# Optimization experiments

Measured on AMD Instinct MI355X. Metric: run time of the kernel, lower is better.

## Reference

```python
import jax, jax.numpy as jnp
import numpy as np

BS, N, HID, INPUT, PREK, KHOP = 16, 1024, 64, 64, 4, 3
D = 2 * HID            # hidden channel dim (128)
F = 2 * INPUT          # input feature dim (128)
C = F + D              # graphconv input channels (256)
NM = KHOP + 1          # num_metrics = k_hop*n_supports + 1 with n_supports=1
PI = 3.141592653589793
EMB_RANGE = (12.0 + 2.0) / HID   # (gamma + epsilon) / hidden_size


def setup_inputs() -> dict:
    key = jax.random.key(0)
    ks = jax.random.split(key, 12)
    inputs = jax.random.normal(ks[0], (BS, N, F), jnp.float32)
    # per-sample dynamic support; scale by 1/N to keep Chebyshev recursion stable
    supports = jax.random.uniform(ks[1], (BS, N, N), jnp.float32) / N
    hidden_states = jax.random.normal(ks[2], (BS, PREK, N, D), jnp.float32)
    W = jax.random.normal(ks[3], (D, D), jnp.float32) * 0.02
    b = jax.random.normal(ks[4], (N, D), jnp.float32) * 0.02
    R = jax.random.normal(ks[5], (PREK, N, HID), jnp.float32) * 0.02
    gc_w = jax.random.normal(ks[6], (D, C * NM), jnp.float32) * 0.02
    gc_b = jax.random.normal(ks[7], (D,), jnp.float32) * 0.02
    ev_att_w = jax.random.normal(ks[8], (1, N * D), jnp.float32) * 0.001
    ev_att_b = jax.random.normal(ks[9], (1,), jnp.float32) * 0.02
    att_w = jax.random.normal(ks[10], (1, N * D), jnp.float32) * 0.001
    att_b = jax.random.normal(ks[11], (1,), jnp.float32) * 0.02
    return {"inputs": inputs, "supports": supports, "hidden_states": hidden_states,
            "W": W, "b": b, "R": R, "gc_w": gc_w, "gc_b": gc_b,
            "ev_att_w": ev_att_w, "ev_att_b": ev_att_b,
            "att_w": att_w, "att_b": att_b}


def reference(inputs, supports, hidden_states, W, b, R, gc_w, gc_b,
              ev_att_w, ev_att_b, att_w, att_b):
    bs, k, n, d = hidden_states.shape
    # split inputs / last hidden into real/imag halves
    re_in, im_in = jnp.split(inputs, 2, axis=-1)          # [bs,n,INPUT]
    preH = hidden_states[:, -1]                           # [bs,n,d]
    re_p, im_p = jnp.split(preH, 2, axis=-1)              # [bs,n,HID]
    conv_in = jnp.concatenate([re_in, re_p, im_in, im_p], axis=-1)  # [bs,n,C]

    # diffusion graph conv (Chebyshev-style recursion over single batched support)
    x0 = conv_in
    x1 = jnp.matmul(supports, x0)                         # [bs,n,C]
    xs = [x0, x1]
    for _ in range(2, KHOP + 1):
        x2 = 2.0 * jnp.matmul(supports, x1) - x0
        xs.append(x2)
        x0, x1 = x1, x2
    # stack K metrics, permute to [bs,n,C,K], flatten (channel-major, step-minor)
    x = jnp.stack(xs, axis=0).transpose(1, 2, 3, 0).reshape(bs, n, C * NM)
    gco = x @ gc_w.T + gc_b                               # [bs,n,d]

    # EvolutionCell attention over g=1 group (kept for faithfulness)
    xe = gco.reshape(bs, 1, n * d)
    se = xe @ ev_att_w.T + ev_att_b                       # [bs,1,1]
    we = jax.nn.softmax(se, axis=1)
    conv_out = (xe * we).sum(axis=1).reshape(bs, n, d)

    # leaky_relu_ (slope 0.01)
    conv_out = jnp.where(conv_out >= 0, conv_out, 0.01 * conv_out)

    # RotatE-style complex phase rotation of hidden states
    phase = R / (EMB_RANGE / PI)                          # [k,n,HID]
    re_rel, im_rel = jnp.cos(phase), jnp.sin(phase)
    re_h, im_h = jnp.split(hidden_states, 2, axis=-1)     # [bs,k,n,HID]
    re_new = re_rel * re_h - im_rel * im_h
    im_new = im_rel * re_h + re_rel * im_h
    new_states = jnp.concatenate([re_new, im_new], axis=-1)  # [bs,k,n,d]

    # attention over k memory slots
    xa = new_states.reshape(bs, k, n * d)
    sa = xa @ att_w.T + att_b                             # [bs,k,1]
    wa = jax.nn.softmax(sa, axis=1)
    att = (xa * wa).sum(axis=1).reshape(bs, n, d)

    output = conv_out @ W + b[None] + att                 # [bs,n,d]
    new_hidden = jnp.concatenate([hidden_states[:, 1:], output[:, None]], axis=1)
    return output, new_hidden
```

## Files before the change

### kernel.cpp

```cpp
#include <hip/hip_runtime.h>
#include <cstddef>

constexpr float PHASE_SCALE = (float)(3.141592653589793 / ((12.0 + 2.0) / 64.0));

typedef __bf16 bf16;
typedef __bf16 bf16x4 __attribute__((ext_vector_type(4)));
typedef __bf16 bf16x8 __attribute__((ext_vector_type(8)));
typedef float floatx4 __attribute__((ext_vector_type(4)));

#define GLOAD_LDS16(gp, lp) __builtin_amdgcn_global_load_lds( \
    (const __attribute__((address_space(1))) void*)(gp),      \
    (__attribute__((address_space(3))) void*)(lp), 16, 0, 0)

__global__ __launch_bounds__(256) void prep_kernel(
    const float4* __restrict__ S, bf16* __restrict__ Sbf,
    const float* __restrict__ R,
    const float* __restrict__ gcw, const float* __restrict__ W,
    bf16* __restrict__ gtAll, bf16* __restrict__ WT,
    const float* __restrict__ inp, const float* __restrict__ hs,
    bf16* __restrict__ xRow, bf16* __restrict__ xT0,
    const float* __restrict__ attw, float* __restrict__ part)
{
    __shared__ bf16 tile[64][65];
    __shared__ float red[256];
    const int bid = blockIdx.x;
    const int tid = threadIdx.x;

    if (bid < 576) {
        int gi = bid * 256 + tid;
        if (gi < 131072) {
            int m = gi >> 15;
            int rem = gi & 32767;
            int d = rem >> 8;
            int c = rem & 255;
            gtAll[gi] = (bf16)gcw[(size_t)d * 1024 + c * 4 + m];
        } else {
            int r = gi - 131072;
            int n = r >> 7, k = r & 127;
            WT[r] = (bf16)W[(size_t)k * 128 + n];
        }
    } else if (bid < 1088) {
        int bid3 = bid - 576;
        int bk = bid3 & 63;
        int k = bk & 3;
        int chunk = bid3 >> 6;
        const float* hbase = hs + (size_t)bk * 131072;
        float acc = 0.f;
        for (int idx = tid; idx < 2048; idx += 256) {
            int h4 = (idx & 15) * 4;
            int n = chunk * 128 + (idx >> 4);
            float4 rr  = *(const float4*)(R + (size_t)k * 65536 + n * 64 + h4);
            float4 re  = *(const float4*)(hbase + (size_t)n * 128 + h4);
            float4 im  = *(const float4*)(hbase + (size_t)n * 128 + 64 + h4);
            float4 wre = *(const float4*)(attw + (size_t)n * 128 + h4);
            float4 wim = *(const float4*)(attw + (size_t)n * 128 + 64 + h4);
            float sv, cv;
            __sincosf(rr.x * PHASE_SCALE, &sv, &cv);
            acc += (cv * re.x - sv * im.x) * wre.x + (sv * re.x + cv * im.x) * wim.x;
            __sincosf(rr.y * PHASE_SCALE, &sv, &cv);
            acc += (cv * re.y - sv * im.y) * wre.y + (sv * re.y + cv * im.y) * wim.y;
            __sincosf(rr.z * PHASE_SCALE, &sv, &cv);
            acc += (cv * re.z - sv * im.z) * wre.z + (sv * re.z + cv * im.z) * wim.z;
            __sincosf(rr.w * PHASE_SCALE, &sv, &cv);
            acc += (cv * re.w - sv * im.w) * wre.w + (sv * re.w + cv * im.w) * wim.w;
        }
        red[tid] = acc;
        __syncthreads();
        for (int s2 = 128; s2 > 0; s2 >>= 1) {
            if (tid < s2) red[tid] += red[tid + s2];
            __syncthreads();
        }
        if (tid == 0) part[bk * 8 + chunk] = red[0];
    } else if (bid < 2112) {
        int bid2 = bid - 1088;
        int b = bid2 >> 6;
        int by = (bid2 >> 2) & 15;
        int bx = bid2 & 3;
        int n0 = by * 64, c0 = bx * 64;
        #pragma unroll
        for (int it = 0; it < 16; ++it) {
            int idx = it * 256 + tid;
            int cl = idx & 63, nl = idx >> 6;
            int n = n0 + nl, c = c0 + cl;
            const float* irow = inp + ((size_t)b * 1024 + n) * 128;
            const float* prow = hs + (((size_t)b * 4 + 3) * 1024 + n) * 128;
            float v;
            if (c < 64)       v = irow[c];
            else if (c < 128) v = prow[c - 64];
            else if (c < 192) v = irow[c - 64];
            else              v = prow[c - 128];
            bf16 vb = (bf16)v;
            xRow[((size_t)b * 1024 + n) * 256 + c] = vb;
            tile[nl][cl] = vb;
        }
        __syncthreads();
        #pragma unroll
        for (int it = 0; it < 16; ++it) {
            int idx = it * 256 + tid;
            int nl = idx & 63, cl = idx >> 6;
            xT0[((size_t)b * 256 + c0 + cl) * 1024 + n0 + nl] = tile[nl][cl];
        }
    } else {
        int gi = (bid - 2112) * 256 + tid;
        const float4* Sp = S + (size_t)gi * 2;
        float4 v0 = Sp[0];
        float4 v1 = Sp[1];
        bf16x8 o;
        o[0] = (bf16)v0.x; o[1] = (bf16)v0.y; o[2] = (bf16)v0.z; o[3] = (bf16)v0.w;
        o[4] = (bf16)v1.x; o[5] = (bf16)v1.y; o[6] = (bf16)v1.z; o[7] = (bf16)v1.w;
        *(bf16x8*)(Sbf + (size_t)gi * 8) = o;
    }
}

__global__ __launch_bounds__(512) void cheb_mfma_kernel(
    const bf16* __restrict__ S, const bf16* __restrict__ xT,
    const bf16* __restrict__ xTprev, bf16* __restrict__ outT,
    const bf16* __restrict__ xRow0, const bf16* __restrict__ gtA,
    const bf16* __restrict__ gt0, float* __restrict__ gcoF,
    float alpha, int accumulate)
{
    __shared__ char smem[81920];
    const int f = blockIdx.x;
    const int b = (f & 7) + 8 * ((f >> 3) & 1);
    const int n0 = (f >> 4) * 64;
    const int tid = threadIdx.x;
    const int wave = tid >> 6, lane = tid & 63;
    const int wr = (wave & 3) * 16;
    const int wc = (wave >> 2) * 128;
    const int l15 = lane & 15, quad = lane >> 4;
    const int lrow = lane >> 3;
    const int segsw = (lane & 7) ^ lrow;

    const bf16* Sb = S + (size_t)b * 1048576;
    const bf16* xb = xT + (size_t)b * 262144;

    auto stage = [&](int p, int k0) {
        bf16* dA = (bf16*)(smem + p * 40960);
        bf16* dB = dA + 4096;
        {
            const bf16* gp = Sb + (size_t)(n0 + wave * 8 + lrow) * 1024 + k0 + segsw * 8;
            GLOAD_LDS16(gp, dA + wave * 8 * 64);
        }
        #pragma unroll
        for (int v = 0; v < 4; ++v) {
            int cq = wave * 32 + v * 8;
            const bf16* gp = xb + (size_t)(cq + lrow) * 1024 + k0 + segsw * 8;
            GLOAD_LDS16(gp, dB + cq * 64);
        }
    };

    floatx4 acc[8] = {};
    stage(0, 0);
    int p = 0;
    for (int k0 = 0; k0 < 1024; k0 += 64) {
        __syncthreads();
        if (k0 + 64 < 1024) stage(p ^ 1, k0 + 64);
        const bf16* lA = (const bf16*)(smem + p * 40960);
        const bf16* lB = lA + 4096;
        #pragma unroll
        for (int ks = 0; ks < 2; ++ks) {
            int row = wr + l15;
            int aslot = (ks * 4 + quad) ^ (row & 7);
            bf16x8 af = *(const bf16x8*)(lA + row * 64 + aslot * 8);
            #pragma unroll
            for (int j = 0; j < 8; ++j) {
                int col = wc + j * 16 + l15;
                int bslot = (ks * 4 + quad) ^ (col & 7);
                bf16x8 bfr = *(const bf16x8*)(lB + col * 64 + bslot * 8);
                acc[j] = __builtin_amdgcn_mfma_f32_16x16x32_bf16(af, bfr, acc[j], 0, 0, 0);
            }
        }
        p ^= 1;
    }

    const bf16* pT = xTprev ? xTprev + (size_t)b * 262144 : nullptr;
    bf16* oT = outT ? outT + (size_t)b * 262144 : nullptr;
    bf16x4 xo[8];
    #pragma unroll
    for (int j = 0; j < 8; ++j) {
        int col = wc + j * 16 + l15;
        float v[4];
        #pragma unroll
        for (int r = 0; r < 4; ++r) v[r] = alpha * acc[j][r];
        if (pT) {
            bf16x4 pp = *(const bf16x4*)(pT + (size_t)col * 1024 + n0 + wr + quad * 4);
            #pragma unroll
            for (int r = 0; r < 4; ++r) v[r] -= (float)pp[r];
        }
        #pragma unroll
        for (int r = 0; r < 4; ++r) xo[j][r] = (bf16)v[r];
        if (oT) *(bf16x4*)(oT + (size_t)col * 1024 + n0 + wr + quad * 4) = xo[j];
    }

    __syncthreads();
    bf16* ldsX = (bf16*)smem;
    #pragma unroll
    for (int j = 0; j < 8; ++j) {
        int col = wc + j * 16 + l15;
        #pragma unroll
        for (int r = 0; r < 4; ++r)
            ldsX[(wr + quad * 4 + r) * 264 + col] = xo[j][r];
    }
    __syncthreads();

    const int dbase = (wave >> 2) * 64;
    floatx4 a2[4] = {};
    for (int k2 = 0; k2 < 256; k2 += 32) {
        bf16x8 af = *(const bf16x8*)(ldsX + (wr + l15) * 264 + k2 + quad * 8);
        #pragma unroll
        for (int j = 0; j < 4; ++j) {
            int dcol = dbase + j * 16 + l15;
            bf16x8 bfr = *(const bf16x8*)(gtA + (size_t)dcol * 256 + k2 + quad * 8);
            a2[j] = __builtin_amdgcn_mfma_f32_16x16x32_bf16(af, bfr, a2[j], 0, 0, 0);
        }
    }
    if (xRow0) {
        for (int k2 = 0; k2 < 256; k2 += 32) {
            bf16x8 af = *(const bf16x8*)(xRow0 + ((size_t)b * 1024 + n0 + wr + l15) * 256 + k2 + quad * 8);
            #pragma unroll
            for (int j = 0; j < 4; ++j) {
                int dcol = dbase + j * 16 + l15;
                bf16x8 bfr = *(const bf16x8*)(gt0 + (size_t)dcol * 256 + k2 + quad * 8);
                a2[j] = __builtin_amdgcn_mfma_f32_16x16x32_bf16(af, bfr, a2[j], 0, 0, 0);
            }
        }
    }
    #pragma unroll
    for (int j = 0; j < 4; ++j) {
        int dcol = dbase + j * 16 + l15;
        #pragma unroll
        for (int r = 0; r < 4; ++r) {
            size_t idx = ((size_t)b * 1024 + n0 + wr + quad * 4 + r) * 128 + dcol;
            if (accumulate) gcoF[idx] += a2[j][r];
            else            gcoF[idx]  = a2[j][r];
        }
    }
}

__global__ __launch_bounds__(256) void final_kernel(
    const float* __restrict__ gcoF, const float* __restrict__ gcb,
    const bf16* __restrict__ WT, const float* __restrict__ bvec,
    const float* __restrict__ hs, const float* __restrict__ R,
    const float* __restrict__ part, const float* __restrict__ attb,
    float* __restrict__ out, float* __restrict__ newh)
{
    const int m0 = blockIdx.x * 64;
    const int b = m0 >> 10, n0 = m0 & 1023;
    const int tid = threadIdx.x;
    const int wave = tid >> 6, lane = tid & 63;
    const int l15 = lane & 15, quad = lane >> 4;

    const int arow = m0 + wave * 16 + l15;
    floatx4 acc[8] = {};
    #pragma unroll
    for (int k0 = 0; k0 < 128; k0 += 32) {
        int kk = k0 + quad * 8;
        float4 p0 = *(const float4*)(gcoF + (size_t)arow * 128 + kk);
        float4 p1 = *(const float4*)(gcoF + (size_t)arow * 128 + kk + 4);
        float4 g0 = *(const float4*)(gcb + kk);
        float4 g1 = *(const float4*)(gcb + kk + 4);
        float vv[8] = {p0.x + g0.x, p0.y + g0.y, p0.z + g0.z, p0.w + g0.w,
                       p1.x + g1.x, p1.y + g1.y, p1.z + g1.z, p1.w + g1.w};
        bf16x8 af;
        #pragma unroll
        for (int e = 0; e < 8; ++e) {
            float v = vv[e];
            af[e] = (bf16)(v >= 0.f ? v : 0.01f * v);
        }
        #pragma unroll
        for (int j = 0; j < 8; ++j) {
            bf16x8 bfr = *(const bf16x8*)(WT + (size_t)(j * 16 + l15) * 128 + kk);
            acc[j] = __builtin_amdgcn_mfma_f32_16x16x32_bf16(af, bfr, acc[j], 0, 0, 0);
        }
    }

    float sa[4], mx = -1e30f;
    #pragma unroll
    for (int k = 0; k < 4; ++k) {
        float s = attb[0];
        #pragma unroll
        for (int c = 0; c < 8; ++c) s += part[(b * 4 + k) * 8 + c];
        sa[k] = s;
        mx = fmaxf(mx, s);
    }
    float den = 0.f;
    #pragma unroll
    for (int k = 0; k < 4; ++k) { sa[k] = __expf(sa[k] - mx); den += sa[k]; }
    float inv = 1.f / den;
    #pragma unroll
    for (int k = 0; k < 4; ++k) sa[k] *= inv;

    #pragma unroll
    for (int jj = 0; jj < 4; ++jj) {
        int hcol = jj * 16 + l15;
        #pragma unroll
        for (int r = 0; r < 4; ++r) {
            int n = n0 + wave * 16 + quad * 4 + r;
            float attRe = 0.f, attIm = 0.f;
            #pragma unroll
            for (int k = 0; k < 4; ++k) {
                const float* hb = hs + (((size_t)(b * 4 + k) * 1024 + n) * 128);
                float re = hb[hcol], im = hb[64 + hcol];
                float s, c;
                __sincosf(R[(size_t)k * 65536 + n * 64 + hcol] * PHASE_SCALE, &s, &c);
                attRe += sa[k] * (c * re - s * im);
                attIm += sa[k] * (s * re + c * im);
                if (k >= 1) {
                    size_t nb = (size_t)b * 524288 + (size_t)(k - 1) * 131072 + (size_t)n * 128;
                    newh[nb + hcol] = re;
                    newh[nb + 64 + hcol] = im;
                }
            }
            size_t ob = (size_t)(m0 + wave * 16 + quad * 4 + r) * 128;
            float oRe = acc[jj][r]     + bvec[(size_t)n * 128 + hcol]      + attRe;
            float oIm = acc[jj + 4][r] + bvec[(size_t)n * 128 + 64 + hcol] + attIm;
            out[ob + hcol] = oRe;
            out[ob + 64 + hcol] = oIm;
            size_t nb3 = (size_t)b * 524288 + 393216 + (size_t)n * 128;
            newh[nb3 + hcol] = oRe;
            newh[nb3 + 64 + hcol] = oIm;
        }
    }
}

extern "C" void kernel_launch(void* const* d_in, const int* in_sizes, int n_in,
                              void* d_out, int out_size, void* d_ws, size_t ws_size,
                              hipStream_t stream) {
    const float* inp  = (const float*)d_in[0];
    const float* sup  = (const float*)d_in[1];
    const float* hs   = (const float*)d_in[2];
    const float* W    = (const float*)d_in[3];
    const float* bvec = (const float*)d_in[4];
    const float* R    = (const float*)d_in[5];
    const float* gcw  = (const float*)d_in[6];
    const float* gcb  = (const float*)d_in[7];
    const float* attw = (const float*)d_in[10];
    const float* attb = (const float*)d_in[11];

    float* out  = (float*)d_out;
    float* newh = out + 2097152;
    bf16*  Sbf  = (bf16*)newh;

    char* w = (char*)d_ws;
    bf16*  xT0   = (bf16*)(w);
    bf16*  xT1   = (bf16*)(w + 8388608);
    bf16*  xT2   = (bf16*)(w + 16777216);
    bf16*  xRow  = (bf16*)(w + 25165824);
    float* gcoF  = (float*)(w + 33554432);
    bf16*  gtAll = (bf16*)(w + 41943040);
    bf16*  WT    = (bf16*)(w + 42205184);
    float* part  = (float*)(w + 42237952);

    prep_kernel<<<10304, 256, 0, stream>>>((const float4*)sup, Sbf, R, gcw, W,
                                           gtAll, WT, inp, hs, xRow, xT0, attw, part);

    cheb_mfma_kernel<<<256, 512, 0, stream>>>(Sbf, xT0, nullptr, xT1,
                                              xRow, gtAll + 32768, gtAll, gcoF, 1.0f, 0);
    cheb_mfma_kernel<<<256, 512, 0, stream>>>(Sbf, xT1, xT0, xT2,
                                              nullptr, gtAll + 2 * 32768, nullptr, gcoF, 2.0f, 1);
    cheb_mfma_kernel<<<256, 512, 0, stream>>>(Sbf, xT2, xT1, nullptr,
                                              nullptr, gtAll + 3 * 32768, nullptr, gcoF, 2.0f, 1);

    final_kernel<<<256, 256, 0, stream>>>(gcoF, gcb, WT, bvec, hs, R, part, attb, out, newh);
}
```

Measured before the change: 264.9 us.

## Restructure prep kernel: vectorized concat/transpose, fused S conversion into all blocks

Shrinks the prep kernel grid from 10304 to 2048 blocks. Every block now converts four chunks of the support matrix to bf16, and the concat/transpose, attention-score and weight-conversion roles are interleaved across blocks. The input concat is rewritten to load float4 pairs and store bf16x8 rows, with the transposed write emitted as bf16x4, replacing scalar per-element loads and stores. The aim is better memory coalescing and less launch overhead, at the cost of heavier, less uniform per-block work.

```diff
diff --git a/kernel.cpp b/kernel.cpp
--- a/kernel.cpp
+++ b/kernel.cpp
@@ -26,24 +26,42 @@
     const int bid = blockIdx.x;
     const int tid = threadIdx.x;
 
-    if (bid < 576) {
-        int gi = bid * 256 + tid;
-        if (gi < 131072) {
-            int m = gi >> 15;
-            int rem = gi & 32767;
-            int d = rem >> 8;
-            int c = rem & 255;
-            gtAll[gi] = (bf16)gcw[(size_t)d * 1024 + c * 4 + m];
-        } else {
-            int r = gi - 131072;
-            int n = r >> 7, k = r & 127;
-            WT[r] = (bf16)W[(size_t)k * 128 + n];
-        }
-    } else if (bid < 1088) {
-        int bid3 = bid - 576;
-        int bk = bid3 & 63;
+    const int lin = ((bid >> 4) << 3) | (bid & 7);
+
+    if (((bid >> 3) & 1) == 0) {
+        int b = lin >> 6, by = (lin >> 2) & 15, bx = lin & 3;
+        int n0 = by * 64, c0 = bx * 64;
+        const float* base = (bx & 1) ? (hs + (((size_t)b * 4 + 3) * 1024) * 128)
+                                     : (inp + ((size_t)b * 1024) * 128);
+        int soff = (bx >> 1) * 64;
+        #pragma unroll
+        for (int it = 0; it < 2; ++it) {
+            int unit = it * 256 + tid;
+            int nl = unit >> 3, cs = unit & 7;
+            const float* src = base + (size_t)(n0 + nl) * 128 + soff + cs * 8;
+            float4 a0 = *(const float4*)src;
+            float4 a1 = *(const float4*)(src + 4);
+            bf16x8 o;
+            o[0] = (bf16)a0.x; o[1] = (bf16)a0.y; o[2] = (bf16)a0.z; o[3] = (bf16)a0.w;
+            o[4] = (bf16)a1.x; o[5] = (bf16)a1.y; o[6] = (bf16)a1.z; o[7] = (bf16)a1.w;
+            *(bf16x8*)(xRow + ((size_t)b * 1024 + n0 + nl) * 256 + c0 + cs * 8) = o;
+            #pragma unroll
+            for (int e = 0; e < 8; ++e) tile[nl][cs * 8 + e] = o[e];
+        }
+        __syncthreads();
+        #pragma unroll
+        for (int it = 0; it < 4; ++it) {
+            int unit = it * 256 + tid;
+            int ng = unit & 15, cc = unit >> 4;
+            bf16x4 v;
+            #pragma unroll
+            for (int r = 0; r < 4; ++r) v[r] = tile[ng * 4 + r][cc];
+            *(bf16x4*)(xT0 + ((size_t)b * 256 + c0 + cc) * 1024 + n0 + ng * 4) = v;
+        }
+    } else if (lin < 512) {
+        int bk = lin & 63;
         int k = bk & 3;
-        int chunk = bid3 >> 6;
+        int chunk = lin >> 6;
         const float* hbase = hs + (size_t)bk * 131072;
         float acc = 0.f;
         for (int idx = tid; idx < 2048; idx += 256) {
@@ -71,44 +89,33 @@
             __syncthreads();
         }
         if (tid == 0) part[bk * 8 + chunk] = red[0];
-    } else if (bid < 2112) {
-        int bid2 = bid - 1088;
-        int b = bid2 >> 6;
-        int by = (bid2 >> 2) & 15;
-        int bx = bid2 & 3;
-        int n0 = by * 64, c0 = bx * 64;
-        #pragma unroll
-        for (int it = 0; it < 16; ++it) {
-            int idx = it * 256 + tid;
-            int cl = idx & 63, nl = idx >> 6;
-            int n = n0 + nl, c = c0 + cl;
-            const float* irow = inp + ((size_t)b * 1024 + n) * 128;
-            const float* prow = hs + (((size_t)b * 4 + 3) * 1024 + n) * 128;
-            float v;
-            if (c < 64)       v = irow[c];
-            else if (c < 128) v = prow[c - 64];
-            else if (c < 192) v = irow[c - 64];
-            else              v = prow[c - 128];
-            bf16 vb = (bf16)v;
-            xRow[((size_t)b * 1024 + n) * 256 + c] = vb;
-            tile[nl][cl] = vb;
-        }
-        __syncthreads();
-        #pragma unroll
-        for (int it = 0; it < 16; ++it) {
-            int idx = it * 256 + tid;
-            int nl = idx & 63, cl = idx >> 6;
-            xT0[((size_t)b * 256 + c0 + cl) * 1024 + n0 + nl] = tile[nl][cl];
-        }
     } else {
-        int gi = (bid - 2112) * 256 + tid;
-        const float4* Sp = S + (size_t)gi * 2;
+        int wid = lin - 512;
+        for (int wi = wid * 256 + tid; wi < 147456; wi += 131072) {
+            if (wi < 131072) {
+                int m = wi >> 15;
+                int rem = wi & 32767;
+                int d = rem >> 8;
+                int c = rem & 255;
+                gtAll[wi] = (bf16)gcw[(size_t)d * 1024 + c * 4 + m];
+            } else {
+                int r2 = wi - 131072;
+                int n = r2 >> 7, kx = r2 & 127;
+                WT[r2] = (bf16)W[(size_t)kx * 128 + n];
+            }
+        }
+    }
+
+    #pragma unroll
+    for (int i = 0; i < 4; ++i) {
+        size_t gi = ((size_t)(bid * 4 + i)) * 256 + tid;
+        const float4* Sp = S + gi * 2;
         float4 v0 = Sp[0];
         float4 v1 = Sp[1];
         bf16x8 o;
         o[0] = (bf16)v0.x; o[1] = (bf16)v0.y; o[2] = (bf16)v0.z; o[3] = (bf16)v0.w;
         o[4] = (bf16)v1.x; o[5] = (bf16)v1.y; o[6] = (bf16)v1.z; o[7] = (bf16)v1.w;
-        *(bf16x8*)(Sbf + (size_t)gi * 8) = o;
+        *(bf16x8*)(Sbf + gi * 8) = o;
     }
 }
 
@@ -351,8 +358,8 @@
     bf16*  WT    = (bf16*)(w + 42205184);
     float* part  = (float*)(w + 42237952);
 
-    prep_kernel<<<10304, 256, 0, stream>>>((const float4*)sup, Sbf, R, gcw, W,
-                                           gtAll, WT, inp, hs, xRow, xT0, attw, part);
+    prep_kernel<<<2048, 256, 0, stream>>>((const float4*)sup, Sbf, R, gcw, W,
+                                          gtAll, WT, inp, hs, xRow, xT0, attw, part);
 
     cheb_mfma_kernel<<<256, 512, 0, stream>>>(Sbf, xT0, nullptr, xT1,
                                               xRow, gtAll + 32768, gtAll, gcoF, 1.0f, 0);
```

After: 270.7 us. 2.2% more time.
